# Kernel tuning notes

Hardware: AMD Instinct MI355X
Metric: run time of the kernel (lower is better)

Reference implementation:

```python
import math
import jax, jax.numpy as jnp
import numpy as np

N_HEADS = 8
GROUPS = 32
EPS = 1e-5


def setup_inputs() -> dict:
    key = jax.random.key(0)
    ks = jax.random.split(key, 4)
    B, C, H, W = 8, 512, 32, 32
    x = jax.random.normal(ks[0], (B, C, H, W), dtype=jnp.float32)
    gn_scale = jnp.ones((C,), dtype=jnp.float32)
    gn_bias = jnp.zeros((C,), dtype=jnp.float32)
    # small init so softmax logits stay in a sane range (original zero-inits
    # proj_out; we use small random weights so the output is non-trivial)
    qkv_w = jax.random.normal(ks[1], (3 * C, C), dtype=jnp.float32) * 0.02
    qkv_b = jnp.zeros((3 * C,), dtype=jnp.float32)
    proj_w = jax.random.normal(ks[2], (C, C), dtype=jnp.float32) * 0.02
    proj_b = jnp.zeros((C,), dtype=jnp.float32)
    return {"x": x, "gn_scale": gn_scale, "gn_bias": gn_bias,
            "qkv_w": qkv_w, "qkv_b": qkv_b,
            "proj_w": proj_w, "proj_b": proj_b}


def reference(x, gn_scale, gn_bias, qkv_w, qkv_b, proj_w, proj_b):
    b, c, H, W = x.shape
    L = H * W
    xr = x.reshape(b, c, L)

    # GroupNorm32: normalize in fp32 over (channels_per_group, L)
    xf = xr.astype(jnp.float32).reshape(b, GROUPS, -1)
    mu = xf.mean(axis=-1, keepdims=True)
    var = xf.var(axis=-1, keepdims=True)
    xn = ((xf - mu) * jax.lax.rsqrt(var + EPS)).reshape(b, c, L)
    xn = (xn * gn_scale[:, None] + gn_bias[:, None]).astype(x.dtype)

    # 1x1 conv QKV projection: [b, 3C, L]
    qkv = jnp.einsum('oc,bcl->bol', qkv_w, xn) + qkv_b[:, None]

    # QKVAttentionLegacy: split 3C axis as (heads, 3*ch)
    ch = c // N_HEADS
    qkv = qkv.reshape(b * N_HEADS, 3 * ch, L)
    q, k, v = qkv[:, :ch], qkv[:, ch:2 * ch], qkv[:, 2 * ch:]
    scale = 1.0 / math.sqrt(math.sqrt(ch))
    w = jnp.einsum('bct,bcs->bts', q * scale, k * scale)  # [b*h, L, L]
    w = jax.nn.softmax(w.astype(jnp.float32), axis=-1).astype(qkv.dtype)
    a = jnp.einsum('bts,bcs->bct', w, v).reshape(b, c, L)

    # 1x1 conv output projection + residual
    h = jnp.einsum('oc,bcl->bol', proj_w, a) + proj_b[:, None]
    return (xr + h).reshape(b, c, H, W)
```

## Files before the change

kernel.cpp:

```cpp
#include <hip/hip_runtime.h>
#include <hip/hip_bf16.h>

typedef __attribute__((ext_vector_type(8))) short v8s;
typedef __attribute__((ext_vector_type(8))) unsigned short u16x8;
typedef __attribute__((ext_vector_type(4))) float v4f;
typedef __attribute__((ext_vector_type(16))) float f32x16;

#define MFMA16(a, b, c) __builtin_amdgcn_mfma_f32_16x16x32_bf16((a), (b), (c), 0, 0, 0)
#define MFMA32(a, b, c) __builtin_amdgcn_mfma_f32_32x32x16_bf16((a), (b), (c), 0, 0, 0)

#define GLL16(g, l)                                                        \
  __builtin_amdgcn_global_load_lds(                                        \
      (const __attribute__((address_space(1))) unsigned int*)(g),          \
      (__attribute__((address_space(3))) unsigned int*)(l), 16, 0, 0)

#if __has_builtin(__builtin_amdgcn_exp2f)
__device__ __forceinline__ float exp2n(float x) { return __builtin_amdgcn_exp2f(x); }
#else
__device__ __forceinline__ float exp2n(float x) {
  float r; asm("v_exp_f32 %0, %1" : "=v"(r) : "v"(x)); return r;
}
#endif

__device__ __forceinline__ unsigned short f2bf(float f) {
  union { float f; unsigned u; } v; v.f = f;
  unsigned r = v.u + 0x7fffu + ((v.u >> 16) & 1u);
  return (unsigned short)(r >> 16);
}

__device__ __forceinline__ unsigned cvtpk(float lo, float hi) {
  unsigned r;
  asm("v_cvt_pk_bf16_f32 %0, %1, %2" : "=v"(r) : "v"(lo), "v"(hi));
  return r;
}
__device__ __forceinline__ void pl32swap(unsigned& a, unsigned& b) {
  asm("v_permlane32_swap_b32 %0, %1" : "+v"(a), "+v"(b));
}

__global__ __launch_bounds__(256) void cvt_gn_kernel(const float* __restrict__ in0,
                                                     unsigned short* __restrict__ out0,
                                                     const float* __restrict__ in1,
                                                     unsigned short* __restrict__ out1,
                                                     int n0, int n1,
                                                     const float* __restrict__ x,
                                                     float2* __restrict__ stats) {
  if (blockIdx.x < 1024) {
    int i = blockIdx.x * 256 + threadIdx.x;
    const float* in; unsigned short* out;
    if (i < n0) { in = in0; out = out0; }
    else        { i -= n0; if (i >= n1) return; in = in1; out = out1; }
    float4 v = ((const float4*)in)[i];
    ushort4 o;
    o.x = f2bf(v.x); o.y = f2bf(v.y); o.z = f2bf(v.z); o.w = f2bf(v.w);
    ((ushort4*)out)[i] = o;
    return;
  }
  const int bg = blockIdx.x - 1024;
  const float4* xp4 = (const float4*)(x + (size_t)bg * 16 * 1024);
  float s = 0.f, ss = 0.f;
  for (int i = threadIdx.x; i < 4096; i += 256) {
    float4 v = xp4[i];
    s  += (v.x + v.y) + (v.z + v.w);
    ss += (v.x * v.x + v.y * v.y) + (v.z * v.z + v.w * v.w);
  }
  #pragma unroll
  for (int d = 1; d < 64; d <<= 1) { s += __shfl_xor(s, d); ss += __shfl_xor(ss, d); }
  __shared__ float red[2][4];
  const int w = threadIdx.x >> 6;
  if ((threadIdx.x & 63) == 0) { red[0][w] = s; red[1][w] = ss; }
  __syncthreads();
  if (threadIdx.x == 0) {
    s  = red[0][0] + red[0][1] + red[0][2] + red[0][3];
    ss = red[1][0] + red[1][1] + red[1][2] + red[1][3];
    const float mu  = s * (1.f / 16384.f);
    const float var = ss * (1.f / 16384.f) - mu * mu;
    stats[bg] = make_float2(mu, rsqrtf(var + 1e-5f));
  }
}

__global__ __launch_bounds__(256) void gnt_kernel(const float* __restrict__ x,
                                                  const float2* __restrict__ stats,
                                                  const float* __restrict__ gsc,
                                                  const float* __restrict__ gbi,
                                                  unsigned short* __restrict__ xnT) {
  const int b = blockIdx.z, l0 = blockIdx.x * 64, c0 = blockIdx.y * 64;
  const float* sp = x + (size_t)b * 512 * 1024;
  unsigned short* dp = xnT + (size_t)b * 1024 * 512;
  __shared__ unsigned T[64][65];
  const int tid = threadIdx.x;
  const int rr = tid >> 3, c8 = (tid & 7) * 8;
  #pragma unroll
  for (int sw = 0; sw < 2; ++sw) {
    const int c = c0 + sw * 32 + rr;
    const float2 st = stats[b * 32 + (c >> 4)];
    const float sc = gsc[c] * st.y;
    const float bi = gbi[c] - st.x * sc;
    const float4* px = (const float4*)(sp + (size_t)c * 1024 + l0 + c8);
    float4 v0 = px[0], v1 = px[1];
    T[sw * 32 + rr][c8 + 0] = f2bf(v0.x * sc + bi);
    T[sw * 32 + rr][c8 + 1] = f2bf(v0.y * sc + bi);
    T[sw * 32 + rr][c8 + 2] = f2bf(v0.z * sc + bi);
    T[sw * 32 + rr][c8 + 3] = f2bf(v0.w * sc + bi);
    T[sw * 32 + rr][c8 + 4] = f2bf(v1.x * sc + bi);
    T[sw * 32 + rr][c8 + 5] = f2bf(v1.y * sc + bi);
    T[sw * 32 + rr][c8 + 6] = f2bf(v1.z * sc + bi);
    T[sw * 32 + rr][c8 + 7] = f2bf(v1.w * sc + bi);
  }
  __syncthreads();
  #pragma unroll
  for (int sw = 0; sw < 2; ++sw) {
    const int ll = sw * 32 + rr;
    u16x8 o;
    #pragma unroll
    for (int j = 0; j < 8; ++j) o[j] = (unsigned short)T[c8 + j][ll];
    *(u16x8*)(dp + (size_t)(l0 + ll) * 512 + c0 + c8) = o;
  }
}

template <bool QKV, int NT>
__global__ __launch_bounds__(256) void gemm_kernel(
    const unsigned short* __restrict__ A,
    const unsigned short* __restrict__ BT,
    const float* __restrict__ bias,
    const float* __restrict__ xres,
    float* __restrict__ outf,
    unsigned short* __restrict__ qT,
    unsigned short* __restrict__ kT,
    unsigned short* __restrict__ vO) {
  constexpr int K = 512;
  constexpr int NFR = NT / 32;
  constexpr int NJOB = 16 + NT / 8;
  const int n0 = blockIdx.x * NT, m0 = blockIdx.y * 128, b = blockIdx.z;
  const unsigned short* Bp = BT + (size_t)b * 1024 * K;

  __shared__ __align__(16) unsigned short As[128][64];
  __shared__ __align__(16) unsigned short Bs[NT][64];

  const int tid = threadIdx.x, lane = tid & 63, w = tid >> 6;
  const int quad = lane >> 4, l15 = lane & 15;
  const int wm = (w >> 1) * 64, wn = (w & 1) * (NT / 2);
  const int srow = lane >> 3;
  const int scol = ((lane & 7) ^ srow) * 8;
  const int ck0 = ((quad ^ (l15 & 7)) * 8);
  const int ck1 = ck0 ^ 32;
  const unsigned short* Asf = &As[0][0];
  const unsigned short* Bsf = &Bs[0][0];

  v4f acc[4][NFR];
  #pragma unroll
  for (int i = 0; i < 4; ++i)
    #pragma unroll
    for (int j = 0; j < NFR; ++j) acc[i][j] = (v4f){0.f, 0.f, 0.f, 0.f};

  for (int kk = 0; kk < K; kk += 64) {
    __syncthreads();
    #pragma unroll
    for (int jj = 0; jj < NJOB / 4; ++jj) {
      const int job = w * (NJOB / 4) + jj;
      if (job < 16) {
        GLL16(A + (size_t)(m0 + job * 8 + srow) * K + kk + scol, &As[job * 8][0]);
      } else {
        const int j2 = job - 16;
        GLL16(Bp + (size_t)(n0 + j2 * 8 + srow) * K + kk + scol, &Bs[j2 * 8][0]);
      }
    }
    __syncthreads();
    #pragma unroll
    for (int h = 0; h < 2; ++h) {
      const int ck = h ? ck1 : ck0;
      v8s af[4], bf[NFR];
      #pragma unroll
      for (int mt = 0; mt < 4; ++mt) af[mt] = *(const v8s*)(Asf + (wm + mt * 16 + l15) * 64 + ck);
      #pragma unroll
      for (int nt = 0; nt < NFR; ++nt) bf[nt] = *(const v8s*)(Bsf + (wn + nt * 16 + l15) * 64 + ck);
      #pragma unroll
      for (int mt = 0; mt < 4; ++mt)
        #pragma unroll
        for (int nt = 0; nt < NFR; ++nt)
          acc[mt][nt] = MFMA16(af[mt], bf[nt], acc[mt][nt]);
    }
  }

  if (QKV) {
    const int bh8 = b * 8;
    const float cs = 0.18033688011112042f;
    #pragma unroll
    for (int mt = 0; mt < 4; ++mt) {
      const int m4 = m0 + wm + mt * 16 + quad * 4;
      const int h = m4 / 192;
      const int rr = m4 - h * 192;
      const int part = rr >> 6;
      const int ch = rr & 63;
      const float b0 = bias[m4], b1 = bias[m4 + 1], b2 = bias[m4 + 2], b3 = bias[m4 + 3];
      #pragma unroll
      for (int nt = 0; nt < NFR; ++nt) {
        const int n = n0 + wn + nt * 16 + l15;
        v4f a = acc[mt][nt];
        const float v0 = a[0] + b0, v1 = a[1] + b1, v2 = a[2] + b2, v3 = a[3] + b3;
        if (part == 0) {
          ushort4 st4;
          st4.x = f2bf(v0 * cs); st4.y = f2bf(v1 * cs);
          st4.z = f2bf(v2 * cs); st4.w = f2bf(v3 * cs);
          *(ushort4*)(qT + ((size_t)(bh8 + h) * 1024 + n) * 64 + ch) = st4;
        } else if (part == 1) {
          ushort4 st4;
          st4.x = f2bf(v0); st4.y = f2bf(v1); st4.z = f2bf(v2); st4.w = f2bf(v3);
          *(ushort4*)(kT + ((size_t)(bh8 + h) * 1024 + n) * 64 + ch) = st4;
        } else {
          unsigned short* dp = vO + ((size_t)(bh8 + h) * 64 + ch) * 1024 + n;
          dp[0] = f2bf(v0); dp[1024] = f2bf(v1); dp[2048] = f2bf(v2); dp[3072] = f2bf(v3);
        }
      }
    }
  } else {
    #pragma unroll
    for (int mt = 0; mt < 4; ++mt) {
      const int m4 = m0 + wm + mt * 16 + quad * 4;
      const float b0 = bias[m4], b1 = bias[m4 + 1], b2 = bias[m4 + 2], b3 = bias[m4 + 3];
      #pragma unroll
      for (int nt = 0; nt < NFR; ++nt) {
        const int n = n0 + wn + nt * 16 + l15;
        const size_t i0 = ((size_t)b * 512 + m4) * 1024 + n;
        outf[i0]        = xres[i0]        + acc[mt][nt][0] + b0;
        outf[i0 + 1024] = xres[i0 + 1024] + acc[mt][nt][1] + b1;
        outf[i0 + 2048] = xres[i0 + 2048] + acc[mt][nt][2] + b2;
        outf[i0 + 3072] = xres[i0 + 3072] + acc[mt][nt][3] + b3;
      }
    }
  }
}

__global__ __launch_bounds__(256) void attn_kernel(const unsigned short* __restrict__ qT,
                                                   const unsigned short* __restrict__ kT,
                                                   const unsigned short* __restrict__ vv,
                                                   unsigned short* __restrict__ aT) {
  const int bh = blockIdx.x;
  const int t0 = blockIdx.y * 256;
  const unsigned short* qb = qT + (size_t)bh * 1024 * 64;
  const unsigned short* kb = kT + (size_t)bh * 1024 * 64;
  const unsigned short* vb = vv + (size_t)bh * 64 * 1024;

  __shared__ __align__(16) unsigned short Ks[2][128][64];
  __shared__ __align__(16) unsigned short Vs[2][2][64][64];

  const int tid = threadIdx.x, w = tid >> 6, lane = tid & 63;
  const int l31 = lane & 31, h = lane >> 5;
  const int srow = lane >> 3;
  const int scol = ((lane & 7) ^ srow) * 8;

  #pragma unroll
  for (int jj = 0; jj < 8; ++jj) {
    const int seg = w * 8 + jj;
    GLL16(qb + (size_t)(t0 + seg * 8 + srow) * 64 + scol, &Ks[0][0][0] + seg * 8 * 64);
  }
  __syncthreads();
  v8s qf[2][4];
  #pragma unroll
  for (int tb = 0; tb < 2; ++tb) {
    const int row = w * 64 + tb * 32 + l31;
    const unsigned short* qr = &Ks[0][0][0] + row * 64;
    const int rx = row & 7;
    #pragma unroll
    for (int kb2 = 0; kb2 < 4; ++kb2)
      qf[tb][kb2] = *(const v8s*)(qr + ((kb2 * 2 + h) ^ rx) * 8);
  }
  __syncthreads();

  #pragma unroll
  for (int jj = 0; jj < 8; ++jj) {
    const int j = w * 8 + jj;
    if (j < 16) {
      GLL16(kb + (size_t)(j * 8 + srow) * 64 + scol, &Ks[0][j * 8][0]);
    } else {
      const int j2 = j - 16, hf = j2 >> 3, cg = (j2 & 7) * 8;
      GLL16(vb + (size_t)(cg + srow) * 1024 + hf * 64 + scol, &Vs[0][hf][cg][0]);
    }
  }

  f32x16 o[2][2];
  #pragma unroll
  for (int tb = 0; tb < 2; ++tb)
    #pragma unroll
    for (int cb = 0; cb < 2; ++cb)
      #pragma unroll
      for (int r = 0; r < 16; ++r) o[tb][cb][r] = 0.f;
  float lsum[2] = {0.f, 0.f};

  for (int it = 0; it < 8; ++it) {
    __syncthreads();
    if (it + 1 < 8) {
      const int s1 = (it + 1) * 128, bp1 = (it + 1) & 1;
      #pragma unroll
      for (int jj = 0; jj < 8; ++jj) {
        const int j = w * 8 + jj;
        if (j < 16) {
          GLL16(kb + (size_t)(s1 + j * 8 + srow) * 64 + scol, &Ks[bp1][j * 8][0]);
        } else {
          const int j2 = j - 16, hf = j2 >> 3, cg = (j2 & 7) * 8;
          GLL16(vb + (size_t)(cg + srow) * 1024 + s1 + hf * 64 + scol,
                &Vs[bp1][hf][cg][0]);
        }
      }
    }
    const int buf = it & 1;

    #pragma unroll
    for (int hf = 0; hf < 2; ++hf) {
      const unsigned short* Kb = &Ks[buf][hf * 64][0];
      const unsigned short* Vb = &Vs[buf][hf][0][0];

      v8s kf[2][4], vf[2][4];
      #pragma unroll
      for (int sb = 0; sb < 2; ++sb) {
        const int row = sb * 32 + l31, rx = row & 7;
        const unsigned short* kr = Kb + row * 64;
        #pragma unroll
        for (int kb2 = 0; kb2 < 4; ++kb2)
          kf[sb][kb2] = *(const v8s*)(kr + ((kb2 * 2 + h) ^ rx) * 8);
      }
      #pragma unroll
      for (int cb = 0; cb < 2; ++cb) {
        const int row = cb * 32 + l31, rx = row & 7;
        const unsigned short* vr = Vb + row * 64;
        #pragma unroll
        for (int i = 0; i < 4; ++i)
          vf[cb][i] = *(const v8s*)(vr + ((i * 2 + h) ^ rx) * 8);
      }

      #pragma unroll
      for (int tb = 0; tb < 2; ++tb) {
        #pragma unroll
        for (int sb = 0; sb < 2; ++sb) {
          f32x16 sa = {0.f,0.f,0.f,0.f,0.f,0.f,0.f,0.f,0.f,0.f,0.f,0.f,0.f,0.f,0.f,0.f};
          #pragma unroll
          for (int kb2 = 0; kb2 < 4; ++kb2)
            sa = MFMA32(kf[sb][kb2], qf[tb][kb2], sa);
          float p[16]; float rsum = 0.f;
          #pragma unroll
          for (int r = 0; r < 16; ++r) { p[r] = exp2n(sa[r]); rsum += p[r]; }
          lsum[tb] += rsum;
          unsigned c0 = cvtpk(p[0], p[1]),  c1 = cvtpk(p[2], p[3]);
          unsigned c2 = cvtpk(p[4], p[5]),  c3 = cvtpk(p[6], p[7]);
          pl32swap(c0, c2); pl32swap(c1, c3);
          unsigned c4 = cvtpk(p[8], p[9]),  c5 = cvtpk(p[10], p[11]);
          unsigned c6 = cvtpk(p[12], p[13]), c7 = cvtpk(p[14], p[15]);
          pl32swap(c4, c6); pl32swap(c5, c7);
          union { v8s v; unsigned u[4]; } pa0, pa1;
          pa0.u[0] = c0; pa0.u[1] = c1; pa0.u[2] = c2; pa0.u[3] = c3;
          pa1.u[0] = c4; pa1.u[1] = c5; pa1.u[2] = c6; pa1.u[3] = c7;
          #pragma unroll
          for (int cb = 0; cb < 2; ++cb) {
            o[tb][cb] = MFMA32(pa0.v, vf[cb][sb * 2 + 0], o[tb][cb]);
            o[tb][cb] = MFMA32(pa1.v, vf[cb][sb * 2 + 1], o[tb][cb]);
          }
        }
      }
    }
  }

  const int b = bh >> 3, hd = bh & 7;
  #pragma unroll
  for (int tb = 0; tb < 2; ++tb) {
    lsum[tb] += __shfl_xor(lsum[tb], 32);
    #pragma unroll
    for (int r = 0; r < 16; ++r) {
      const int trow = (r & 3) + 8 * (r >> 2) + 4 * h;
      const float inv = 1.0f / __shfl(lsum[tb], trow);
      const int t = t0 + w * 64 + tb * 32 + trow;
      unsigned short* dst = aT + ((size_t)b * 1024 + t) * 512 + hd * 64;
      dst[l31]      = f2bf(o[tb][0][r] * inv);
      dst[32 + l31] = f2bf(o[tb][1][r] * inv);
    }
  }
}

extern "C" void kernel_launch(void* const* d_in, const int* in_sizes, int n_in,
                              void* d_out, int out_size, void* d_ws, size_t ws_size,
                              hipStream_t stream) {
  const float* x    = (const float*)d_in[0];
  const float* gsc  = (const float*)d_in[1];
  const float* gbi  = (const float*)d_in[2];
  const float* qkvw = (const float*)d_in[3];
  const float* qkvb = (const float*)d_in[4];
  const float* pjw  = (const float*)d_in[5];
  const float* pjb  = (const float*)d_in[6];
  float* out = (float*)d_out;

  unsigned short* ws  = (unsigned short*)d_ws;
  unsigned short* qw  = ws;
  unsigned short* pw  = qw + 786432;
  float2* stats = (float2*)(pw + 262144);
  unsigned short* xnT = pw + 262144 + 1024;
  unsigned short* qT  = xnT + 4194304;
  unsigned short* kT  = qT + 4194304;
  unsigned short* vv  = kT + 4194304;
  unsigned short* aT  = vv + 4194304;

  cvt_gn_kernel<<<dim3(1280), dim3(256), 0, stream>>>(qkvw, qw, pjw, pw, 196608, 65536,
                                                      x, stats);
  gnt_kernel<<<dim3(16, 8, 8), dim3(256), 0, stream>>>(x, stats, gsc, gbi, xnT);
  gemm_kernel<true, 128><<<dim3(8, 12, 8), dim3(256), 0, stream>>>(
      qw, xnT, qkvb, nullptr, nullptr, qT, kT, vv);
  attn_kernel<<<dim3(64, 4), dim3(256), 0, stream>>>(qT, kT, vv, aT);
  gemm_kernel<false, 64><<<dim3(16, 4, 8), dim3(256), 0, stream>>>(
      pw, aT, pjb, x, out, nullptr, nullptr, nullptr);
}
```

Before: 148.6 us.

## Fuse GroupNorm statistics with normalize-transpose kernel using LDS-cached group tile

The GroupNorm statistics pass now stages each (batch, group) slab of x in shared memory, reduces mean and variance in-block, and then writes the normalized bf16 transposed activations directly. This removes the separate normalize-transpose kernel, one launch, and the second global read of x. In exchange each block reserves 64KB of LDS, including the weight-conversion blocks, which limits occupancy. The transposed stores are strided 16-byte writes, and only 256 blocks do the normalization work.

```diff
diff --git a/kernel.cpp b/kernel.cpp
--- a/kernel.cpp
+++ b/kernel.cpp
@@ -43,7 +43,10 @@
                                                      unsigned short* __restrict__ out1,
                                                      int n0, int n1,
                                                      const float* __restrict__ x,
-                                                     float2* __restrict__ stats) {
+                                                     const float* __restrict__ gsc,
+                                                     const float* __restrict__ gbi,
+                                                     unsigned short* __restrict__ xnT) {
+  __shared__ __align__(16) float xsf[16384];
   if (blockIdx.x < 1024) {
     int i = blockIdx.x * 256 + threadIdx.x;
     const float* in; unsigned short* out;
@@ -56,64 +59,56 @@
     return;
   }
   const int bg = blockIdx.x - 1024;
-  const float4* xp4 = (const float4*)(x + (size_t)bg * 16 * 1024);
+  const int b = bg >> 5, g = bg & 31;
+  const int tid = threadIdx.x;
+  const float4* xp4 = (const float4*)(x + (size_t)bg * 16384);
+  float4* xs4 = (float4*)xsf;
   float s = 0.f, ss = 0.f;
-  for (int i = threadIdx.x; i < 4096; i += 256) {
+  #pragma unroll
+  for (int k = 0; k < 16; ++k) {
+    const int i = k * 256 + tid;
     float4 v = xp4[i];
+    xs4[i] = v;
     s  += (v.x + v.y) + (v.z + v.w);
     ss += (v.x * v.x + v.y * v.y) + (v.z * v.z + v.w * v.w);
   }
   #pragma unroll
   for (int d = 1; d < 64; d <<= 1) { s += __shfl_xor(s, d); ss += __shfl_xor(ss, d); }
-  __shared__ float red[2][4];
-  const int w = threadIdx.x >> 6;
-  if ((threadIdx.x & 63) == 0) { red[0][w] = s; red[1][w] = ss; }
-  __syncthreads();
-  if (threadIdx.x == 0) {
-    s  = red[0][0] + red[0][1] + red[0][2] + red[0][3];
-    ss = red[1][0] + red[1][1] + red[1][2] + red[1][3];
-    const float mu  = s * (1.f / 16384.f);
-    const float var = ss * (1.f / 16384.f) - mu * mu;
-    stats[bg] = make_float2(mu, rsqrtf(var + 1e-5f));
-  }
-}
-
-__global__ __launch_bounds__(256) void gnt_kernel(const float* __restrict__ x,
-                                                  const float2* __restrict__ stats,
-                                                  const float* __restrict__ gsc,
-                                                  const float* __restrict__ gbi,
-                                                  unsigned short* __restrict__ xnT) {
-  const int b = blockIdx.z, l0 = blockIdx.x * 64, c0 = blockIdx.y * 64;
-  const float* sp = x + (size_t)b * 512 * 1024;
-  unsigned short* dp = xnT + (size_t)b * 1024 * 512;
-  __shared__ unsigned T[64][65];
-  const int tid = threadIdx.x;
-  const int rr = tid >> 3, c8 = (tid & 7) * 8;
-  #pragma unroll
-  for (int sw = 0; sw < 2; ++sw) {
-    const int c = c0 + sw * 32 + rr;
-    const float2 st = stats[b * 32 + (c >> 4)];
-    const float sc = gsc[c] * st.y;
-    const float bi = gbi[c] - st.x * sc;
-    const float4* px = (const float4*)(sp + (size_t)c * 1024 + l0 + c8);
-    float4 v0 = px[0], v1 = px[1];
-    T[sw * 32 + rr][c8 + 0] = f2bf(v0.x * sc + bi);
-    T[sw * 32 + rr][c8 + 1] = f2bf(v0.y * sc + bi);
-    T[sw * 32 + rr][c8 + 2] = f2bf(v0.z * sc + bi);
-    T[sw * 32 + rr][c8 + 3] = f2bf(v0.w * sc + bi);
-    T[sw * 32 + rr][c8 + 4] = f2bf(v1.x * sc + bi);
-    T[sw * 32 + rr][c8 + 5] = f2bf(v1.y * sc + bi);
-    T[sw * 32 + rr][c8 + 6] = f2bf(v1.z * sc + bi);
-    T[sw * 32 + rr][c8 + 7] = f2bf(v1.w * sc + bi);
-  }
-  __syncthreads();
-  #pragma unroll
-  for (int sw = 0; sw < 2; ++sw) {
-    const int ll = sw * 32 + rr;
-    u16x8 o;
-    #pragma unroll
-    for (int j = 0; j < 8; ++j) o[j] = (unsigned short)T[c8 + j][ll];
-    *(u16x8*)(dp + (size_t)(l0 + ll) * 512 + c0 + c8) = o;
+  __syncthreads();
+  float save = 0.f;
+  if (tid < 10) save = xsf[tid];
+  __syncthreads();
+  if ((tid & 63) == 0) { xsf[(tid >> 6) * 2] = s; xsf[(tid >> 6) * 2 + 1] = ss; }
+  __syncthreads();
+  if (tid == 0) {
+    const float S  = xsf[0] + xsf[2] + xsf[4] + xsf[6];
+    const float SS = xsf[1] + xsf[3] + xsf[5] + xsf[7];
+    const float mu  = S * (1.f / 16384.f);
+    const float var = SS * (1.f / 16384.f) - mu * mu;
+    xsf[8] = mu; xsf[9] = rsqrtf(var + 1e-5f);
+  }
+  __syncthreads();
+  const float mu = xsf[8], rs = xsf[9];
+  __syncthreads();
+  if (tid < 10) xsf[tid] = save;
+  __syncthreads();
+  float scv[16], biv[16];
+  #pragma unroll
+  for (int j = 0; j < 16; ++j) {
+    scv[j] = gsc[g * 16 + j] * rs;
+    biv[j] = gbi[g * 16 + j] - mu * scv[j];
+  }
+  unsigned short* dp = xnT + (size_t)b * 1024 * 512 + g * 16;
+  #pragma unroll
+  for (int k = 0; k < 4; ++k) {
+    const int l = k * 256 + tid;
+    u16x8 o0, o1;
+    #pragma unroll
+    for (int j = 0; j < 8; ++j) o0[j] = f2bf(xsf[j * 1024 + l] * scv[j] + biv[j]);
+    #pragma unroll
+    for (int j = 0; j < 8; ++j) o1[j] = f2bf(xsf[(8 + j) * 1024 + l] * scv[8 + j] + biv[8 + j]);
+    *(u16x8*)(dp + (size_t)l * 512)     = o0;
+    *(u16x8*)(dp + (size_t)l * 512 + 8) = o1;
   }
 }
 
@@ -389,7 +384,6 @@
   unsigned short* ws  = (unsigned short*)d_ws;
   unsigned short* qw  = ws;
   unsigned short* pw  = qw + 786432;
-  float2* stats = (float2*)(pw + 262144);
   unsigned short* xnT = pw + 262144 + 1024;
   unsigned short* qT  = xnT + 4194304;
   unsigned short* kT  = qT + 4194304;
@@ -397,8 +391,7 @@
   unsigned short* aT  = vv + 4194304;
 
   cvt_gn_kernel<<<dim3(1280), dim3(256), 0, stream>>>(qkvw, qw, pjw, pw, 196608, 65536,
-                                                      x, stats);
-  gnt_kernel<<<dim3(16, 8, 8), dim3(256), 0, stream>>>(x, stats, gsc, gbi, xnT);
+                                                      x, gsc, gbi, xnT);
   gemm_kernel<true, 128><<<dim3(8, 12, 8), dim3(256), 0, stream>>>(
       qw, xnT, qkvb, nullptr, nullptr, qT, kT, vv);
   attn_kernel<<<dim3(64, 4), dim3(256), 0, stream>>>(qT, kT, vv, aT);
```

Result: faster. 143.4 us (-3.5%).
